# Kernel optimization log

Measured on AMD Instinct MI355X. Metric: run time of the kernel, lower is better.

The kernel has to match this reference:

```python
import jax, jax.numpy as jnp
import numpy as np

N = 50000      # nodes
E = 800000     # edges
D_IN = 128
D_OUT = 128


def setup_inputs() -> dict:
    key = jax.random.key(0)
    k1, k2, k3 = jax.random.split(key, 3)
    x = jax.random.normal(k1, (N, D_IN), dtype=jnp.float32)
    edge_index = jax.random.randint(k2, (2, E), 0, N, dtype=jnp.int32)
    W = jax.random.normal(k3, (D_OUT, D_IN), dtype=jnp.float32) / np.sqrt(D_IN)
    b = jnp.zeros((D_OUT,), dtype=jnp.float32)
    return {"x": x, "edge_index": edge_index, "W": W, "b": b}


def reference(x, edge_index, W, b):
    # PyG GCNConv: add self-loops, symmetric D^{-1/2}(A+I)D^{-1/2} normalization,
    # linear transform, scatter-sum aggregation, then bias.
    n = x.shape[0]
    loop = jnp.arange(n, dtype=edge_index.dtype)
    src = jnp.concatenate([edge_index[0], loop])  # [E+N]
    dst = jnp.concatenate([edge_index[1], loop])  # [E+N]

    # degree over destination nodes (incl. self-loops)
    deg = jax.ops.segment_sum(jnp.ones_like(dst, dtype=x.dtype), dst, num_segments=n)
    dinv = jnp.where(deg > 0, jax.lax.rsqrt(deg), 0.0)
    norm = dinv[src] * dinv[dst]                  # [E+N]

    x_lin = x @ W.T                               # [N, D_OUT]
    msgs = x_lin[src] * norm[:, None]             # gather + scale, [E+N, D_OUT]
    out = jax.ops.segment_sum(msgs, dst, num_segments=n)  # scatter-add
    return out + b
```

## Files before the change

kernel.cpp:

```cpp
#include <hip/hip_runtime.h>
#include <math.h>

#define D_FEAT 128
#define NB1 391
#define EPB 2048
#define NBUCK 782
#define NPB 64
#define SUBCAP 24
#define ELDS 1536
#define CSTRIDE 1664

__device__ __forceinline__ unsigned short bf16_rne(float f) {
    unsigned int u = __float_as_uint(f);
    u += 0x7FFFu + ((u >> 16) & 1u);
    return (unsigned short)(u >> 16);
}

#define TK 64
#define LP 64
__global__ __launch_bounds__(256) void build_gemm_kernel(
    const int* __restrict__ src, const int* __restrict__ dst,
    unsigned int* __restrict__ subbuck, unsigned short* __restrict__ cnt_sub,
    int E, int n,
    const float* __restrict__ A, const float* __restrict__ W,
    unsigned short* __restrict__ y) {
    if (blockIdx.x < NB1) {
        __shared__ int hist[NBUCK];
        int t = threadIdx.x;
        int B = blockIdx.x;
        for (int j = t; j < NBUCK; j += 256) hist[j] = 0;
        __syncthreads();
        int base = B * EPB;
        int bk[8], r[8];
        unsigned int pk[8];
        bool v[8];
#pragma unroll
        for (int j = 0; j < 8; ++j) {
            int e = base + j * 256 + t;
            v[j] = e < E;
            int d = v[j] ? dst[e] : 0;
            int s = v[j] ? src[e] : 0;
            bk[j] = d >> 6;
            pk[j] = ((unsigned int)(d & 63) << 16) | (unsigned int)s;
        }
#pragma unroll
        for (int j = 0; j < 8; ++j)
            r[j] = v[j] ? atomicAdd(&hist[bk[j]], 1) : 0;
        __syncthreads();
        for (int j = t; j < NBUCK; j += 256)
            cnt_sub[(size_t)B * NBUCK + j] = (unsigned short)min(hist[j], SUBCAP);
#pragma unroll
        for (int j = 0; j < 8; ++j)
            if (v[j] && r[j] < SUBCAP)
                subbuck[((size_t)bk[j] * NB1 + B) * SUBCAP + r[j]] = pk[j];
        return;
    }

    int bb = blockIdx.x - NB1;
    __shared__ float As[TK * LP];
    __shared__ float Bs[TK * LP];
    int t = threadIdx.x;
    int r0 = (bb >> 1) * 64;
    int c0 = (bb & 1) * 64;
    int tx = t & 15;
    int ty = t >> 4;
    int lrow = t >> 2;
    int lk = (t & 3) * 16;

    float acc[4][4];
#pragma unroll
    for (int i = 0; i < 4; ++i)
#pragma unroll
        for (int j = 0; j < 4; ++j) acc[i][j] = 0.0f;

    int grow = r0 + lrow;
    const float* Ap = A + (size_t)grow * D_FEAT + lk;
    const float* Wp = W + (size_t)(c0 + lrow) * D_FEAT + lk;

    for (int kk = 0; kk < D_FEAT; kk += TK) {
#pragma unroll
        for (int j = 0; j < 4; ++j) {
            float4 av = (grow < n) ? *(const float4*)(Ap + kk + j * 4)
                                   : make_float4(0.f, 0.f, 0.f, 0.f);
            float4 wv = *(const float4*)(Wp + kk + j * 4);
            int kb = lk + j * 4;
            As[(kb + 0) * LP + lrow] = av.x;
            As[(kb + 1) * LP + lrow] = av.y;
            As[(kb + 2) * LP + lrow] = av.z;
            As[(kb + 3) * LP + lrow] = av.w;
            Bs[(kb + 0) * LP + lrow] = wv.x;
            Bs[(kb + 1) * LP + lrow] = wv.y;
            Bs[(kb + 2) * LP + lrow] = wv.z;
            Bs[(kb + 3) * LP + lrow] = wv.w;
        }
        __syncthreads();
#pragma unroll 8
        for (int k = 0; k < TK; ++k) {
            float4 a = *(const float4*)&As[k * LP + ty * 4];
            float4 b = *(const float4*)&Bs[k * LP + tx * 4];
            acc[0][0] += a.x * b.x; acc[0][1] += a.x * b.y;
            acc[0][2] += a.x * b.z; acc[0][3] += a.x * b.w;
            acc[1][0] += a.y * b.x; acc[1][1] += a.y * b.y;
            acc[1][2] += a.y * b.z; acc[1][3] += a.y * b.w;
            acc[2][0] += a.z * b.x; acc[2][1] += a.z * b.y;
            acc[2][2] += a.z * b.z; acc[2][3] += a.z * b.w;
            acc[3][0] += a.w * b.x; acc[3][1] += a.w * b.y;
            acc[3][2] += a.w * b.z; acc[3][3] += a.w * b.w;
        }
        __syncthreads();
    }

#pragma unroll
    for (int i = 0; i < 4; ++i) {
        int row = r0 + ty * 4 + i;
        if (row < n) {
            ushort4 o;
            o.x = bf16_rne(acc[i][0]);
            o.y = bf16_rne(acc[i][1]);
            o.z = bf16_rne(acc[i][2]);
            o.w = bf16_rne(acc[i][3]);
            *(ushort4*)(y + (size_t)row * D_FEAT + c0 + tx * 4) = o;
        }
    }
}

__global__ __launch_bounds__(256) void bin_kernel(
    const unsigned int* __restrict__ subbuck,
    const unsigned short* __restrict__ cnt_sub,
    unsigned short* __restrict__ csr, uint4* __restrict__ meta,
    float* __restrict__ dinv, int n) {
    __shared__ unsigned int eds[ELDS];
    __shared__ int sarr[512];
    __shared__ int hist[NPB];
    __shared__ int p2[NPB];
    __shared__ int cur[NPB];
    int b = blockIdx.x, t = threadIdx.x;

    int c0 = (t < NB1) ? (int)cnt_sub[(size_t)t * NBUCK + b] : 0;
    int c1 = (t + 256 < NB1) ? (int)cnt_sub[(size_t)(t + 256) * NBUCK + b] : 0;
    sarr[t] = c0;
    sarr[t + 256] = c1;
    if (t < NPB) hist[t] = 0;
    __syncthreads();
    for (int ofs = 1; ofs < 512; ofs <<= 1) {
        int u0 = (t >= ofs) ? sarr[t - ofs] : 0;
        int u1 = (t + 256 >= ofs) ? sarr[t + 256 - ofs] : 0;
        __syncthreads();
        sarr[t] += u0;
        sarr[t + 256] += u1;
        __syncthreads();
    }
    int M = sarr[511];
    if (M > ELDS) M = ELDS;

    {
        int sb = sarr[t] - c0;
        const unsigned int* sp = subbuck + ((size_t)b * NB1 + t) * SUBCAP;
        for (int j = 0; j < c0; ++j)
            if (sb + j < ELDS) eds[sb + j] = sp[j];
    }
    if (t + 256 < NB1) {
        int sb = sarr[t + 256] - c1;
        const unsigned int* sp = subbuck + ((size_t)b * NB1 + t + 256) * SUBCAP;
        for (int j = 0; j < c1; ++j)
            if (sb + j < ELDS) eds[sb + j] = sp[j];
    }
    __syncthreads();

    for (int e = t; e < M; e += 256) atomicAdd(&hist[eds[e] >> 16], 1);
    __syncthreads();

    int node = b * NPB + t;
    bool vn = (t < NPB) && (node < n);
    int deg = (t < NPB) ? hist[t] : 0;
    int tot = vn ? deg + 1 : 0;
    if (t < NPB) sarr[t] = tot;
    __syncthreads();
    for (int ofs = 1; ofs < NPB; ofs <<= 1) {
        int u = (t < NPB && t >= ofs) ? sarr[t - ofs] : 0;
        __syncthreads();
        if (t < NPB) sarr[t] += u;
        __syncthreads();
    }
    if (t < NPB) {
        int pb = sarr[t] - tot;
        p2[t] = pb;
        cur[t] = 0;
        if (vn) {
            int start = b * CSTRIDE + pb;
            float dv = rsqrtf((float)(deg + 1));
            meta[node] = make_uint4((unsigned int)start, (unsigned int)tot,
                                    __float_as_uint(dv), 0u);
            dinv[node] = dv;
            csr[start] = (unsigned short)node;
        }
    }
    __syncthreads();

    for (int e = t; e < M; e += 256) {
        int loc = eds[e] >> 16;
        int sl = atomicAdd(&cur[loc], 1);
        csr[b * CSTRIDE + p2[loc] + 1 + sl] = (unsigned short)(eds[e] & 0xffffu);
    }
}

__global__ __launch_bounds__(256) void agg_kernel(const unsigned short* __restrict__ y,
                                                  const float* __restrict__ dinv,
                                                  const uint4* __restrict__ meta,
                                                  const unsigned short* __restrict__ csr,
                                                  const float* __restrict__ bias,
                                                  float* __restrict__ out, int n) {
    int lane = threadIdx.x & 63;
    int wv = threadIdx.x >> 6;
    int i = blockIdx.x * 4 + wv;
    if (i >= n) return;

    uint4 m = meta[i];
    int start = (int)m.x;
    int tot = (int)m.y;
    float di = __uint_as_float(m.z);
    int tot64 = min(tot, 64);

    int ent = (lane < tot64) ? (int)csr[start + lane] : 0;
    float wgt = (lane < tot64) ? dinv[ent] * di : 0.f;

    int g = lane >> 4;
    int sl = lane & 15;

    float acc[8];
#pragma unroll
    for (int k = 0; k < 8; ++k) acc[k] = 0.f;

    const uint4* yq = (const uint4*)y;
    for (int e = 0; e < tot64; e += 8) {
        int i0 = e + g, i1 = e + 4 + g;
        int s0 = __shfl(ent, min(i0, 63), 64);
        int s1 = __shfl(ent, min(i1, 63), 64);
        float w0s = __shfl(wgt, min(i0, 63), 64);
        float w1s = __shfl(wgt, min(i1, 63), 64);
        float w0 = (i0 < tot64) ? w0s : 0.f;
        float w1 = (i1 < tot64) ? w1s : 0.f;
        uint4 q0 = yq[(size_t)s0 * 16 + sl];
        uint4 q1 = yq[(size_t)s1 * 16 + sl];
        acc[0] += __uint_as_float(q0.x << 16) * w0;
        acc[1] += __uint_as_float(q0.x & 0xffff0000u) * w0;
        acc[2] += __uint_as_float(q0.y << 16) * w0;
        acc[3] += __uint_as_float(q0.y & 0xffff0000u) * w0;
        acc[4] += __uint_as_float(q0.z << 16) * w0;
        acc[5] += __uint_as_float(q0.z & 0xffff0000u) * w0;
        acc[6] += __uint_as_float(q0.w << 16) * w0;
        acc[7] += __uint_as_float(q0.w & 0xffff0000u) * w0;
        acc[0] += __uint_as_float(q1.x << 16) * w1;
        acc[1] += __uint_as_float(q1.x & 0xffff0000u) * w1;
        acc[2] += __uint_as_float(q1.y << 16) * w1;
        acc[3] += __uint_as_float(q1.y & 0xffff0000u) * w1;
        acc[4] += __uint_as_float(q1.z << 16) * w1;
        acc[5] += __uint_as_float(q1.z & 0xffff0000u) * w1;
        acc[6] += __uint_as_float(q1.w << 16) * w1;
        acc[7] += __uint_as_float(q1.w & 0xffff0000u) * w1;
    }
    for (int e = 64; e < tot; e += 8) {
        int i0 = e + g, i1 = e + 4 + g;
        int s0 = (i0 < tot) ? (int)csr[start + i0] : 0;
        int s1 = (i1 < tot) ? (int)csr[start + i1] : 0;
        float w0 = (i0 < tot) ? dinv[s0] * di : 0.f;
        float w1 = (i1 < tot) ? dinv[s1] * di : 0.f;
        uint4 q0 = yq[(size_t)s0 * 16 + sl];
        uint4 q1 = yq[(size_t)s1 * 16 + sl];
        acc[0] += __uint_as_float(q0.x << 16) * w0;
        acc[1] += __uint_as_float(q0.x & 0xffff0000u) * w0;
        acc[2] += __uint_as_float(q0.y << 16) * w0;
        acc[3] += __uint_as_float(q0.y & 0xffff0000u) * w0;
        acc[4] += __uint_as_float(q0.z << 16) * w0;
        acc[5] += __uint_as_float(q0.z & 0xffff0000u) * w0;
        acc[6] += __uint_as_float(q0.w << 16) * w0;
        acc[7] += __uint_as_float(q0.w & 0xffff0000u) * w0;
        acc[0] += __uint_as_float(q1.x << 16) * w1;
        acc[1] += __uint_as_float(q1.x & 0xffff0000u) * w1;
        acc[2] += __uint_as_float(q1.y << 16) * w1;
        acc[3] += __uint_as_float(q1.y & 0xffff0000u) * w1;
        acc[4] += __uint_as_float(q1.z << 16) * w1;
        acc[5] += __uint_as_float(q1.z & 0xffff0000u) * w1;
        acc[6] += __uint_as_float(q1.w << 16) * w1;
        acc[7] += __uint_as_float(q1.w & 0xffff0000u) * w1;
    }

#pragma unroll
    for (int k = 0; k < 8; ++k) {
        acc[k] += __shfl_xor(acc[k], 16, 64);
        acc[k] += __shfl_xor(acc[k], 32, 64);
    }

    if (lane < 16) {
        const float4* b4 = (const float4*)bias;
        float4 bv0 = b4[sl * 2], bv1 = b4[sl * 2 + 1];
        float4* op = (float4*)(out + (size_t)i * D_FEAT + sl * 8);
        op[0] = make_float4(acc[0] + bv0.x, acc[1] + bv0.y, acc[2] + bv0.z, acc[3] + bv0.w);
        op[1] = make_float4(acc[4] + bv1.x, acc[5] + bv1.y, acc[6] + bv1.z, acc[7] + bv1.w);
    }
}

extern "C" void kernel_launch(void* const* d_in, const int* in_sizes, int n_in,
                              void* d_out, int out_size, void* d_ws, size_t ws_size,
                              hipStream_t stream) {
    const float* x = (const float*)d_in[0];
    const int* ei = (const int*)d_in[1];
    const float* W = (const float*)d_in[2];
    const float* b = (const float*)d_in[3];
    float* out = (float*)d_out;

    int n = in_sizes[0] / D_FEAT;
    int E = in_sizes[1] / 2;
    const int* src = ei;
    const int* dst = ei + E;

    char* ws = (char*)d_ws;
    size_t off = 0;
    auto alloc = [&](size_t bytes) {
        char* p = ws + off;
        off = (off + bytes + 255) & ~(size_t)255;
        return p;
    };
    unsigned int* subbuck = (unsigned int*)alloc((size_t)NBUCK * NB1 * SUBCAP * 4);
    unsigned short* cnt_sub = (unsigned short*)alloc((size_t)NB1 * NBUCK * 2);
    unsigned short* csr = (unsigned short*)alloc((size_t)NBUCK * CSTRIDE * 2);
    uint4* meta = (uint4*)alloc((size_t)n * 16);
    float* dinv = (float*)alloc((size_t)n * 4);
    unsigned short* y = (unsigned short*)alloc((size_t)n * D_FEAT * 2);
    (void)ws_size;

    int gemm_blocks = ((n + 63) / 64) * 2;
    build_gemm_kernel<<<NB1 + gemm_blocks, 256, 0, stream>>>(
        src, dst, subbuck, cnt_sub, E, n, x, W, y);
    bin_kernel<<<NBUCK, 256, 0, stream>>>(subbuck, cnt_sub, csr, meta, dinv, n);
    agg_kernel<<<(n + 3) / 4, 256, 0, stream>>>(y, dinv, meta, csr, b, out, n);
}
```

Before: 153.2 us.

## Use split-bf16 MFMA for the dense transform GEMM

Replaces the FP32 scalar-FMA shared-memory GEMM with MFMA bf16 16x16x32 instructions. Each FP32 operand is split into hi and lo bf16 parts, and three products (hi*hi, lo*hi, hi*lo) approximate FP32 accuracy. W is split into LDS once per block, and X rows are loaded straight into registers. The goal is to cut GEMM compute time. The cost is three MFMAs per tile plus the split arithmetic, and a slight loss of accuracy from dropping the lo*lo term.

```diff
diff --git a/kernel.cpp b/kernel.cpp
--- a/kernel.cpp
+++ b/kernel.cpp
@@ -10,22 +10,47 @@
 #define ELDS 1536
 #define CSTRIDE 1664
 
+typedef unsigned int u32;
+typedef __bf16 bf16x8 __attribute__((ext_vector_type(8)));
+typedef float f32x4 __attribute__((ext_vector_type(4)));
+
 __device__ __forceinline__ unsigned short bf16_rne(float f) {
     unsigned int u = __float_as_uint(f);
     u += 0x7FFFu + ((u >> 16) & 1u);
     return (unsigned short)(u >> 16);
 }
 
-#define TK 64
-#define LP 64
+__device__ __forceinline__ void split_pack(float a, float b, u32& hi, u32& lo) {
+    u32 ua = __float_as_uint(a), ub = __float_as_uint(b);
+    u32 ha = ua & 0xffff0000u, hb = ub & 0xffff0000u;
+    float ra = a - __uint_as_float(ha);
+    float rb = b - __uint_as_float(hb);
+    hi = hb | (ua >> 16);
+    lo = (__float_as_uint(rb) & 0xffff0000u) | (__float_as_uint(ra) >> 16);
+}
+
+__device__ __forceinline__ void split8(const float4& f0, const float4& f1,
+                                       uint4& hi, uint4& lo) {
+    split_pack(f0.x, f0.y, hi.x, lo.x);
+    split_pack(f0.z, f0.w, hi.y, lo.y);
+    split_pack(f1.x, f1.y, hi.z, lo.z);
+    split_pack(f1.z, f1.w, hi.w, lo.w);
+}
+
+__device__ __forceinline__ f32x4 mfma_bf16(uint4 a, uint4 b, f32x4 c) {
+    return __builtin_amdgcn_mfma_f32_16x16x32_bf16(
+        __builtin_bit_cast(bf16x8, a), __builtin_bit_cast(bf16x8, b), c, 0, 0, 0);
+}
+
 __global__ __launch_bounds__(256) void build_gemm_kernel(
     const int* __restrict__ src, const int* __restrict__ dst,
     unsigned int* __restrict__ subbuck, unsigned short* __restrict__ cnt_sub,
     int E, int n,
     const float* __restrict__ A, const float* __restrict__ W,
     unsigned short* __restrict__ y) {
+    __shared__ u32 smem[2 * 64 * 68];
     if (blockIdx.x < NB1) {
-        __shared__ int hist[NBUCK];
+        int* hist = (int*)smem;
         int t = threadIdx.x;
         int B = blockIdx.x;
         for (int j = t; j < NBUCK; j += 256) hist[j] = 0;
@@ -57,69 +82,75 @@
     }
 
     int bb = blockIdx.x - NB1;
-    __shared__ float As[TK * LP];
-    __shared__ float Bs[TK * LP];
     int t = threadIdx.x;
     int r0 = (bb >> 1) * 64;
     int c0 = (bb & 1) * 64;
-    int tx = t & 15;
-    int ty = t >> 4;
-    int lrow = t >> 2;
-    int lk = (t & 3) * 16;
-
-    float acc[4][4];
-#pragma unroll
-    for (int i = 0; i < 4; ++i)
-#pragma unroll
-        for (int j = 0; j < 4; ++j) acc[i][j] = 0.0f;
-
-    int grow = r0 + lrow;
-    const float* Ap = A + (size_t)grow * D_FEAT + lk;
-    const float* Wp = W + (size_t)(c0 + lrow) * D_FEAT + lk;
-
-    for (int kk = 0; kk < D_FEAT; kk += TK) {
-#pragma unroll
-        for (int j = 0; j < 4; ++j) {
-            float4 av = (grow < n) ? *(const float4*)(Ap + kk + j * 4)
-                                   : make_float4(0.f, 0.f, 0.f, 0.f);
-            float4 wv = *(const float4*)(Wp + kk + j * 4);
-            int kb = lk + j * 4;
-            As[(kb + 0) * LP + lrow] = av.x;
-            As[(kb + 1) * LP + lrow] = av.y;
-            As[(kb + 2) * LP + lrow] = av.z;
-            As[(kb + 3) * LP + lrow] = av.w;
-            Bs[(kb + 0) * LP + lrow] = wv.x;
-            Bs[(kb + 1) * LP + lrow] = wv.y;
-            Bs[(kb + 2) * LP + lrow] = wv.z;
-            Bs[(kb + 3) * LP + lrow] = wv.w;
-        }
-        __syncthreads();
-#pragma unroll 8
-        for (int k = 0; k < TK; ++k) {
-            float4 a = *(const float4*)&As[k * LP + ty * 4];
-            float4 b = *(const float4*)&Bs[k * LP + tx * 4];
-            acc[0][0] += a.x * b.x; acc[0][1] += a.x * b.y;
-            acc[0][2] += a.x * b.z; acc[0][3] += a.x * b.w;
-            acc[1][0] += a.y * b.x; acc[1][1] += a.y * b.y;
-            acc[1][2] += a.y * b.z; acc[1][3] += a.y * b.w;
-            acc[2][0] += a.z * b.x; acc[2][1] += a.z * b.y;
-            acc[2][2] += a.z * b.z; acc[2][3] += a.z * b.w;
-            acc[3][0] += a.w * b.x; acc[3][1] += a.w * b.y;
-            acc[3][2] += a.w * b.z; acc[3][3] += a.w * b.w;
-        }
-        __syncthreads();
-    }
-
-#pragma unroll
-    for (int i = 0; i < 4; ++i) {
-        int row = r0 + ty * 4 + i;
-        if (row < n) {
-            ushort4 o;
-            o.x = bf16_rne(acc[i][0]);
-            o.y = bf16_rne(acc[i][1]);
-            o.z = bf16_rne(acc[i][2]);
-            o.w = bf16_rne(acc[i][3]);
-            *(ushort4*)(y + (size_t)row * D_FEAT + c0 + tx * 4) = o;
+    u32* Whi = smem;
+    u32* Wlo = smem + 64 * 68;
+
+    for (int i = t; i < 1024; i += 256) {
+        int c = i >> 4;
+        int kg = (i & 15) * 8;
+        const float* wp = W + (size_t)(c0 + c) * D_FEAT + kg;
+        float4 f0 = *(const float4*)wp;
+        float4 f1 = *(const float4*)(wp + 4);
+        uint4 hi, lo;
+        split8(f0, f1, hi, lo);
+        int idx = c * 68 + (i & 15) * 4;
+        *(uint4*)&Whi[idx] = hi;
+        *(uint4*)&Wlo[idx] = lo;
+    }
+    __syncthreads();
+
+    int lane = t & 63;
+    int wv = t >> 6;
+    int mrow = r0 + wv * 16 + (lane & 15);
+    bool valid = mrow < n;
+    int kb = (lane >> 4) * 8;
+
+    uint4 xhiu[4], xlou[4];
+    const float* xp = A + (size_t)mrow * D_FEAT + kb;
+#pragma unroll
+    for (int kt = 0; kt < 4; ++kt) {
+        float4 a0, a1;
+        if (valid) {
+            a0 = *(const float4*)(xp + kt * 32);
+            a1 = *(const float4*)(xp + kt * 32 + 4);
+        } else {
+            a0 = make_float4(0.f, 0.f, 0.f, 0.f);
+            a1 = make_float4(0.f, 0.f, 0.f, 0.f);
+        }
+        split8(a0, a1, xhiu[kt], xlou[kt]);
+    }
+
+    f32x4 acc[4];
+#pragma unroll
+    for (int nt = 0; nt < 4; ++nt) acc[nt] = (f32x4){0.f, 0.f, 0.f, 0.f};
+
+#pragma unroll
+    for (int kt = 0; kt < 4; ++kt) {
+        uint4 xh = xhiu[kt], xl = xlou[kt];
+#pragma unroll
+        for (int nt = 0; nt < 4; ++nt) {
+            int idx = (nt * 16 + (lane & 15)) * 68 + kt * 16 + (lane >> 4) * 4;
+            uint4 wh = *(const uint4*)&Whi[idx];
+            uint4 wl = *(const uint4*)&Wlo[idx];
+            acc[nt] = mfma_bf16(wh, xh, acc[nt]);
+            acc[nt] = mfma_bf16(wl, xh, acc[nt]);
+            acc[nt] = mfma_bf16(wh, xl, acc[nt]);
+        }
+    }
+
+    if (valid) {
+        unsigned short* yp = y + (size_t)mrow * D_FEAT + c0 + (lane >> 4) * 4;
+#pragma unroll
+        for (int nt = 0; nt < 4; ++nt) {
+            u32 w0 = (u32)bf16_rne(acc[nt][0]) | ((u32)bf16_rne(acc[nt][1]) << 16);
+            u32 w1 = (u32)bf16_rne(acc[nt][2]) | ((u32)bf16_rne(acc[nt][3]) << 16);
+            uint2 o;
+            o.x = w0;
+            o.y = w1;
+            *(uint2*)(yp + nt * 16) = o;
         }
     }
 }
```

New measurement: 140.2 us. -8.5%, faster.
